# Kernel optimization log

Measured on AMD Instinct MI355X. Metric: run time of the kernel, lower is better.

Reference implementation:

```python
import jax, jax.numpy as jnp
import numpy as np

N, E, G = 50000, 800000, 128
F_IN, H, NHID, C = 310, 128, 64, 2  # H = 2*nhid
NEG_SLOPE = 0.2


def setup_inputs() -> dict:
    key = jax.random.key(0)
    ks = jax.random.split(key, 16)
    def lin(k, fan_in, shape):
        return (jax.random.normal(k, shape, jnp.float32) / np.sqrt(fan_in)).astype(jnp.float32)
    return {
        "x": jax.random.normal(ks[0], (N, F_IN), jnp.float32),
        "edge_index": jax.random.randint(ks[1], (2, E), 0, N, dtype=jnp.int32),
        "batch": jnp.sort(jax.random.randint(ks[2], (N,), 0, G, dtype=jnp.int32)),
        "W1": lin(ks[3], F_IN, (F_IN, H)),
        "a_src1": lin(ks[4], H, (H,)),
        "a_dst1": lin(ks[5], H, (H,)),
        "b1": jnp.zeros((H,), jnp.float32),
        "W2": lin(ks[6], H, (H, H)),
        "a_src2": lin(ks[7], H, (H,)),
        "a_dst2": lin(ks[8], H, (H,)),
        "b2": jnp.zeros((H,), jnp.float32),
        "fc1_w": lin(ks[9], H, (H, NHID)),
        "fc1_b": jnp.zeros((NHID,), jnp.float32),
        "fc2_w": lin(ks[10], NHID, (NHID, C)),
        "fc2_b": jnp.zeros((C,), jnp.float32),
    }


def _gat(x, src, dst, W, a_src, a_dst, b):
    # PyG GATConv, heads=1: h = xW; e_ij = LeakyReLU(a_src.h_j + a_dst.h_i)
    h = x @ W                               # [N, H]
    asrc = h @ a_src                        # [N]
    adst = h @ a_dst                        # [N]
    e = jax.nn.leaky_relu(asrc[src] + adst[dst], NEG_SLOPE)  # [E']
    # segment softmax over incoming edges of each target node
    m = jax.ops.segment_max(e, dst, num_segments=N)
    ex = jnp.exp(e - m[dst])
    s = jax.ops.segment_sum(ex, dst, num_segments=N)
    w = ex / s[dst]                         # [E']
    out = jax.ops.segment_sum(h[src] * w[:, None], dst, num_segments=N)
    return out + b


def reference(x, edge_index, batch, W1, a_src1, a_dst1, b1,
              W2, a_src2, a_dst2, b2, fc1_w, fc1_b, fc2_w, fc2_b):
    # add self loops (GATConv default add_self_loops=True)
    ar = jnp.arange(N, dtype=edge_index.dtype)
    src = jnp.concatenate([edge_index[0], ar])
    dst = jnp.concatenate([edge_index[1], ar])

    h = jax.nn.selu(_gat(x, src, dst, W1, a_src1, a_dst1, b1))
    h = jax.nn.selu(_gat(h, src, dst, W2, a_src2, a_dst2, b2))

    # global mean pool over graphs
    summed = jax.ops.segment_sum(h, batch, num_segments=G)          # [G, H]
    cnt = jax.ops.segment_sum(jnp.ones((N,), h.dtype), batch, num_segments=G)
    pooled = jax.nn.selu(summed / jnp.maximum(cnt, 1.0)[:, None])

    z = jax.nn.selu(pooled @ fc1_w + fc1_b)  # dropout is identity in eval
    logits = z @ fc2_w + fc2_b
    return jax.nn.log_softmax(logits, axis=-1)
```

## Files before the change

kernel.cpp:

```cpp
#include <hip/hip_runtime.h>
#include <hip/hip_bf16.h>
#include <math.h>

#define NN 50000
#define NE 800000
#define NET (NE + NN)
#define FIN 310
#define HD 128
#define NHID 64
#define NCLS 2
#define NG 128
#define NEG_SLOPE 0.2f
#define KP1 320
#define KP2 128

#define SLOTS 64
#define NPART 8
#define PART_SZ (NN / NPART)
#define EPB 4096
#define NSLICE ((NET + EPB - 1) / EPB)

#define SELU_SCALE 1.0507009873554804934193349852946f
#define SELU_ALPHA 1.6732632423543772848170429916717f

typedef short bf16x8 __attribute__((ext_vector_type(8)));
typedef float f32x4 __attribute__((ext_vector_type(4)));

__device__ __forceinline__ float selu(float x) {
    return SELU_SCALE * (x > 0.f ? x : SELU_ALPHA * (expf(x) - 1.f));
}
__device__ __forceinline__ float lrelu(float x) {
    return x > 0.f ? x : NEG_SLOPE * x;
}
__device__ __forceinline__ unsigned short f2bf(float f) {
    unsigned int u = __float_as_uint(f);
    u = (u + 0x7fffu + ((u >> 16) & 1u)) >> 16;
    return (unsigned short)u;
}
__device__ __forceinline__ float bf2f(unsigned short b) {
    return __uint_as_float(((unsigned int)b) << 16);
}


__global__ __launch_bounds__(256) void k_scatter_slots(const int* __restrict__ ei,
                                                       int* __restrict__ cursor,
                                                       int* __restrict__ slots) {
    int part = blockIdx.x & (NPART - 1);
    int slice = blockIdx.x >> 3;
    int lo = part * PART_SZ;
    int base = slice * EPB + threadIdx.x;
#pragma unroll
    for (int k = 0; k < EPB / 256; ++k) {
        int i = base + k * 256;
        if (i >= NET) break;
        int d = (i < NE) ? ei[NE + i] : (i - NE);
        if ((unsigned)(d - lo) < (unsigned)PART_SZ) {
            int s = (i < NE) ? ei[i] : d;
            int pos = atomicAdd(&cursor[d], 1) & (SLOTS - 1);
            slots[(size_t)d * SLOTS + pos] = s;
        }
    }
}


__global__ void k_castT2(const float* __restrict__ W1, const float* __restrict__ W2,
                         unsigned short* __restrict__ W1t, unsigned short* __restrict__ W2t) {
    int i = blockIdx.x * blockDim.x + threadIdx.x;
    const int N1 = HD * KP1;
    if (i < N1) {
        int n = i / KP1, k = i % KP1;
        W1t[i] = (k < FIN) ? f2bf(W1[(size_t)k * HD + n]) : (unsigned short)0;
    } else {
        int j = i - N1;
        if (j < HD * KP2) {
            int n = j / KP2, k = j % KP2;
            W2t[j] = f2bf(W2[(size_t)k * HD + n]);
        }
    }
}


#define GEMM_EPILOGUE                                                          \
    int gr_base = r0 + w * 16 + quad * 4;                                      \
    _Pragma("unroll")                                                          \
    for (int r = 0; r < 4; ++r) {                                              \
        int gr = gr_base + r;                                                  \
        if (gr < M) {                                                          \
            _Pragma("unroll")                                                  \
            for (int nt = 0; nt < 8; ++nt)                                     \
                C[(size_t)gr * HD + nt * 16 + l16] = f2bf(acc[nt][r]);         \
        }                                                                      \
    }                                                                          \
    _Pragma("unroll")                                                          \
    for (int r = 0; r < 4; ++r) {                                              \
        float s1 = 0.f, s2 = 0.f;                                              \
        _Pragma("unroll")                                                      \
        for (int nt = 0; nt < 8; ++nt) {                                       \
            int c = nt * 16 + l16;                                             \
            float v = acc[nt][r];                                              \
            s1 += v * a1s[c];                                                  \
            s2 += v * a2s[c];                                                  \
        }                                                                      \
        _Pragma("unroll")                                                      \
        for (int off = 1; off < 16; off <<= 1) {                               \
            s1 += __shfl_xor(s1, off);                                         \
            s2 += __shfl_xor(s2, off);                                         \
        }                                                                      \
        int gr = gr_base + r;                                                  \
        if (l16 == 0 && gr < M) { asrcp[gr] = s1; adstp[gr] = s2; }            \
    }

__global__ __launch_bounds__(256) void k_gemm_f32(const float* __restrict__ A,
                                                  const unsigned short* __restrict__ Bt,
                                                  unsigned short* __restrict__ C,
                                                  float* __restrict__ asrcp,
                                                  float* __restrict__ adstp,
                                                  const float* __restrict__ a_src,
                                                  const float* __restrict__ a_dst,
                                                  int M, int K, int Kp) {
    __shared__ unsigned short As[64][40];
    __shared__ unsigned short Bs[128][40];
    __shared__ float a1s[HD], a2s[HD];
    int t = threadIdx.x;
    int lane = t & 63, w = t >> 6;
    int quad = lane >> 4, l16 = lane & 15;
    int r0 = blockIdx.x * 64;

    if (t < HD) a1s[t] = a_src[t];
    else a2s[t - HD] = a_dst[t - HD];

    f32x4 acc[8] = {};
    int arow = t >> 4;
    int acol = (t & 15) * 2;
    int brow = t >> 1;
    int bcol = (t & 1) * 16;

    for (int k0 = 0; k0 < Kp; k0 += 32) {
#pragma unroll
        for (int p = 0; p < 4; ++p) {
            int rl = arow + p * 16;
            int gr = r0 + rl;
            int gk = k0 + acol;
            float2 v = make_float2(0.f, 0.f);
            if (gr < M) {
                if (gk + 1 < K) v = *(const float2*)(A + (size_t)gr * K + gk);
                else if (gk < K) v.x = A[(size_t)gr * K + gk];
            }
            ushort2 b;
            b.x = f2bf(v.x); b.y = f2bf(v.y);
            *(ushort2*)&As[rl][acol] = b;
        }
        {
            const unsigned short* src = Bt + (size_t)brow * Kp + k0 + bcol;
            uint4 u0 = *(const uint4*)(src);
            uint4 u1 = *(const uint4*)(src + 8);
            *(uint4*)&Bs[brow][bcol] = u0;
            *(uint4*)&Bs[brow][bcol + 8] = u1;
        }
        __syncthreads();
        bf16x8 af = *(bf16x8*)&As[w * 16 + l16][quad * 8];
#pragma unroll
        for (int nt = 0; nt < 8; ++nt) {
            bf16x8 bfr = *(bf16x8*)&Bs[nt * 16 + l16][quad * 8];
            acc[nt] = __builtin_amdgcn_mfma_f32_16x16x32_bf16(af, bfr, acc[nt], 0, 0, 0);
        }
        __syncthreads();
    }
    GEMM_EPILOGUE
}

__global__ __launch_bounds__(256) void k_gemm_bf16(const unsigned short* __restrict__ A,
                                                   const unsigned short* __restrict__ Bt,
                                                   unsigned short* __restrict__ C,
                                                   float* __restrict__ asrcp,
                                                   float* __restrict__ adstp,
                                                   const float* __restrict__ a_src,
                                                   const float* __restrict__ a_dst,
                                                   int M, int K, int Kp) {
    __shared__ unsigned short As[64][40];
    __shared__ unsigned short Bs[128][40];
    __shared__ float a1s[HD], a2s[HD];
    int t = threadIdx.x;
    int lane = t & 63, w = t >> 6;
    int quad = lane >> 4, l16 = lane & 15;
    int r0 = blockIdx.x * 64;

    if (t < HD) a1s[t] = a_src[t];
    else a2s[t - HD] = a_dst[t - HD];

    f32x4 acc[8] = {};
    int arow = t >> 2;
    int acol = (t & 3) * 8;
    int brow = t >> 1;
    int bcol = (t & 1) * 16;

    for (int k0 = 0; k0 < Kp; k0 += 32) {
        {
            int gr = r0 + arow;
            uint4 v = make_uint4(0, 0, 0, 0);
            if (gr < M) v = *(const uint4*)(A + (size_t)gr * K + k0 + acol);
            *(uint4*)&As[arow][acol] = v;
        }
        {
            const unsigned short* src = Bt + (size_t)brow * Kp + k0 + bcol;
            uint4 u0 = *(const uint4*)(src);
            uint4 u1 = *(const uint4*)(src + 8);
            *(uint4*)&Bs[brow][bcol] = u0;
            *(uint4*)&Bs[brow][bcol + 8] = u1;
        }
        __syncthreads();
        bf16x8 af = *(bf16x8*)&As[w * 16 + l16][quad * 8];
#pragma unroll
        for (int nt = 0; nt < 8; ++nt) {
            bf16x8 bfr = *(bf16x8*)&Bs[nt * 16 + l16][quad * 8];
            acc[nt] = __builtin_amdgcn_mfma_f32_16x16x32_bf16(af, bfr, acc[nt], 0, 0, 0);
        }
        __syncthreads();
    }
    GEMM_EPILOGUE
}


__global__ __launch_bounds__(256) void k_gat(const unsigned short* __restrict__ h,
                                             const float* __restrict__ asrc,
                                             const float* __restrict__ adst,
                                             const int* __restrict__ degv,
                                             const int* __restrict__ slots,
                                             const float* __restrict__ bias,
                                             unsigned short* __restrict__ out) {
    int node = blockIdx.x * 4 + (threadIdx.x >> 6);
    int lane = threadIdx.x & 63;
    if (node >= NN) return;
    int g = lane >> 4, cl = lane & 15;
    int deg = degv[node];
    float adsti = adst[node];

    float acc[8] = {0.f, 0.f, 0.f, 0.f, 0.f, 0.f, 0.f, 0.f};

    int cnt = min(deg, SLOTS);
    int s_c = 0; float p_c = 0.f;
    if (lane < cnt) {
        s_c = slots[(size_t)node * SLOTS + lane];
        p_c = __expf(lrelu(asrc[s_c] + adsti));
    }
    float den_l = p_c;
    int nt = (cnt + 3) >> 2;
    for (int t = 0; t < nt; t += 4) {
        float pv[4]; uint4 hv[4];
#pragma unroll
        for (int u = 0; u < 4; ++u) {
            int tt = t + u;
            bool valid = tt < nt;
            int e = (4 * tt + g) & 63;
            int s = __shfl(s_c, e);
            float p = __shfl(p_c, e);
            int sa = valid ? s : 0;
            pv[u] = valid ? p : 0.f;
            hv[u] = *(const uint4*)(h + (size_t)sa * HD + cl * 8);
        }
#pragma unroll
        for (int u = 0; u < 4; ++u) {
            float p = pv[u];
            unsigned int w0 = hv[u].x, w1 = hv[u].y, w2 = hv[u].z, w3 = hv[u].w;
            acc[0] += p * __uint_as_float(w0 << 16);
            acc[1] += p * __uint_as_float(w0 & 0xffff0000u);
            acc[2] += p * __uint_as_float(w1 << 16);
            acc[3] += p * __uint_as_float(w1 & 0xffff0000u);
            acc[4] += p * __uint_as_float(w2 << 16);
            acc[5] += p * __uint_as_float(w2 & 0xffff0000u);
            acc[6] += p * __uint_as_float(w3 << 16);
            acc[7] += p * __uint_as_float(w3 & 0xffff0000u);
        }
    }
#pragma unroll
    for (int k = 0; k < 8; ++k) {
        acc[k] += __shfl_xor(acc[k], 16);
        acc[k] += __shfl_xor(acc[k], 32);
    }
#pragma unroll
    for (int off = 32; off; off >>= 1)
        den_l += __shfl_xor(den_l, off);

    if (g == 0) {
        float inv = 1.f / den_l;
        int c0 = cl * 8;
        float4 b0 = *(const float4*)(bias + c0);
        float4 b1 = *(const float4*)(bias + c0 + 4);
        float v0 = selu(acc[0] * inv + b0.x);
        float v1 = selu(acc[1] * inv + b0.y);
        float v2 = selu(acc[2] * inv + b0.z);
        float v3 = selu(acc[3] * inv + b0.w);
        float v4 = selu(acc[4] * inv + b1.x);
        float v5 = selu(acc[5] * inv + b1.y);
        float v6 = selu(acc[6] * inv + b1.z);
        float v7 = selu(acc[7] * inv + b1.w);
        uint4 pk;
        pk.x = (unsigned int)f2bf(v0) | ((unsigned int)f2bf(v1) << 16);
        pk.y = (unsigned int)f2bf(v2) | ((unsigned int)f2bf(v3) << 16);
        pk.z = (unsigned int)f2bf(v4) | ((unsigned int)f2bf(v5) << 16);
        pk.w = (unsigned int)f2bf(v6) | ((unsigned int)f2bf(v7) << 16);
        *(uint4*)(out + (size_t)node * HD + c0) = pk;
    }
}


__device__ __forceinline__ int lower_bound_i(const int* a, int n, int key) {
    int lo = 0, hi = n;
    while (lo < hi) {
        int mid = (lo + hi) >> 1;
        if (a[mid] < key) lo = mid + 1; else hi = mid;
    }
    return lo;
}

__global__ __launch_bounds__(512) void k_poolfc(const unsigned short* __restrict__ x,
                                                const int* __restrict__ batch,
                                                const float* __restrict__ w1,
                                                const float* __restrict__ b1,
                                                const float* __restrict__ w2,
                                                const float* __restrict__ b2,
                                                float* __restrict__ out) {
    int g = blockIdx.x;
    int t = threadIdx.x;
    __shared__ int lo_s, hi_s;
    __shared__ float red[512];
    __shared__ float pooled_s[128];
    if (t == 0) {
        lo_s = lower_bound_i(batch, NN, g);
        hi_s = lower_bound_i(batch, NN, g + 1);
    }
    __syncthreads();
    int lo = lo_s, hi = hi_s;
    float acc = 0.f;
    for (int n = lo + (t >> 7); n < hi; n += 4)
        acc += bf2f(x[(size_t)n * HD + (t & 127)]);
    red[t] = acc;
    __syncthreads();
    if (t < 128) {
        float v = red[t] + red[t + 128] + red[t + 256] + red[t + 384];
        pooled_s[t] = selu(v / fmaxf((float)(hi - lo), 1.f));
    }
    __syncthreads();
    if (t < 64) {
        float z = 0.f;
#pragma unroll 8
        for (int k = 0; k < HD; ++k) z += pooled_s[k] * w1[k * NHID + t];
        z = selu(z + b1[t]);
        float p0 = z * w2[t * NCLS + 0];
        float p1 = z * w2[t * NCLS + 1];
        for (int off = 32; off; off >>= 1) {
            p0 += __shfl_down(p0, off);
            p1 += __shfl_down(p1, off);
        }
        if (t == 0) {
            float l0 = p0 + b2[0], l1 = p1 + b2[1];
            float m = fmaxf(l0, l1);
            float lse = m + logf(expf(l0 - m) + expf(l1 - m));
            out[g * NCLS + 0] = l0 - lse;
            out[g * NCLS + 1] = l1 - lse;
        }
    }
}


static inline size_t align_up(size_t v, size_t a) { return (v + a - 1) / a * a; }

extern "C" void kernel_launch(void* const* d_in, const int* in_sizes, int n_in,
                              void* d_out, int out_size, void* d_ws, size_t ws_size,
                              hipStream_t stream) {
    const float* x      = (const float*)d_in[0];
    const int*   ei     = (const int*)d_in[1];
    const int*   batch  = (const int*)d_in[2];
    const float* W1     = (const float*)d_in[3];
    const float* a_src1 = (const float*)d_in[4];
    const float* a_dst1 = (const float*)d_in[5];
    const float* b1     = (const float*)d_in[6];
    const float* W2     = (const float*)d_in[7];
    const float* a_src2 = (const float*)d_in[8];
    const float* a_dst2 = (const float*)d_in[9];
    const float* b2     = (const float*)d_in[10];
    const float* fc1_w  = (const float*)d_in[11];
    const float* fc1_b  = (const float*)d_in[12];
    const float* fc2_w  = (const float*)d_in[13];
    const float* fc2_b  = (const float*)d_in[14];
    float* out = (float*)d_out;

    char* ws = (char*)d_ws;
    size_t off = 0;
    unsigned short* h1 = (unsigned short*)(ws + off); off = align_up(off + (size_t)NN * HD * 2, 256);
    unsigned short* o1 = (unsigned short*)(ws + off); off = align_up(off + (size_t)NN * HD * 2, 256);
    float* asrc = (float*)(ws + off); off = align_up(off + (size_t)NN * 4, 256);
    float* adst = (float*)(ws + off); off = align_up(off + (size_t)NN * 4, 256);
    int* cursor = (int*)(ws + off);   off = align_up(off + (size_t)NN * 4, 256);
    int* slots  = (int*)(ws + off);   off = align_up(off + (size_t)NN * SLOTS * 4, 256);
    unsigned short* W1t = (unsigned short*)(ws + off); off = align_up(off + (size_t)HD * KP1 * 2, 256);
    unsigned short* W2t = (unsigned short*)(ws + off); off = align_up(off + (size_t)HD * KP2 * 2, 256);
    (void)ws_size;

    hipMemsetAsync(cursor, 0, (size_t)NN * 4, stream);
    k_scatter_slots<<<NSLICE * NPART, 256, 0, stream>>>(ei, cursor, slots);

    k_castT2<<<(HD * (KP1 + KP2) + 255) / 256, 256, 0, stream>>>(W1, W2, W1t, W2t);

    int gblocks = (NN + 63) / 64;

    k_gemm_f32<<<gblocks, 256, 0, stream>>>(x, W1t, h1, asrc, adst, a_src1, a_dst1, NN, FIN, KP1);
    k_gat<<<(NN + 3) / 4, 256, 0, stream>>>(h1, asrc, adst, cursor, slots, b1, o1);

    k_gemm_bf16<<<gblocks, 256, 0, stream>>>(o1, W2t, h1, asrc, adst, a_src2, a_dst2, NN, HD, KP2);
    k_gat<<<(NN + 3) / 4, 256, 0, stream>>>(h1, asrc, adst, cursor, slots, b2, o1);

    k_poolfc<<<NG, 512, 0, stream>>>(o1, batch, fc1_w, fc1_b, fc2_w, fc2_b, out);
}
```

Baseline: 315.1 us.

## Shrink GEMM row tile, split columns across waves, narrow GAT unroll, fast math

The GEMM kernels now handle 32 rows per block instead of 64. Each of the four waves covers a 16-row by 64-column quadrant, and the attention dot products are reduced through shared memory. This doubles the block count and halves the accumulator registers, which should raise occupancy. The cost is that each B tile is reused across fewer rows and each block pays an extra barrier. The GAT gather loop is also unrolled by 2 instead of 4 with float2 accumulators, and selu/log-softmax switch to fast __expf/__logf intrinsics, trading a little precision.

```diff
diff --git a/kernel.cpp b/kernel.cpp
--- a/kernel.cpp
+++ b/kernel.cpp
@@ -27,7 +27,7 @@
 typedef float f32x4 __attribute__((ext_vector_type(4)));
 
 __device__ __forceinline__ float selu(float x) {
-    return SELU_SCALE * (x > 0.f ? x : SELU_ALPHA * (expf(x) - 1.f));
+    return SELU_SCALE * (x > 0.f ? x : SELU_ALPHA * (__expf(x) - 1.f));
 }
 __device__ __forceinline__ float lrelu(float x) {
     return x > 0.f ? x : NEG_SLOPE * x;
@@ -81,22 +81,23 @@
 
 
 #define GEMM_EPILOGUE                                                          \
-    int gr_base = r0 + w * 16 + quad * 4;                                      \
+    int rh = w & 1, chf = w >> 1;                                              \
+    int gr_base = r0 + rh * 16 + quad * 4;                                     \
     _Pragma("unroll")                                                          \
     for (int r = 0; r < 4; ++r) {                                              \
         int gr = gr_base + r;                                                  \
         if (gr < M) {                                                          \
             _Pragma("unroll")                                                  \
-            for (int nt = 0; nt < 8; ++nt)                                     \
-                C[(size_t)gr * HD + nt * 16 + l16] = f2bf(acc[nt][r]);         \
+            for (int nt = 0; nt < 4; ++nt)                                     \
+                C[(size_t)gr * HD + chf * 64 + nt * 16 + l16] = f2bf(acc[nt][r]); \
         }                                                                      \
     }                                                                          \
     _Pragma("unroll")                                                          \
     for (int r = 0; r < 4; ++r) {                                              \
         float s1 = 0.f, s2 = 0.f;                                              \
         _Pragma("unroll")                                                      \
-        for (int nt = 0; nt < 8; ++nt) {                                       \
-            int c = nt * 16 + l16;                                             \
+        for (int nt = 0; nt < 4; ++nt) {                                       \
+            int c = chf * 64 + nt * 16 + l16;                                  \
             float v = acc[nt][r];                                              \
             s1 += v * a1s[c];                                                  \
             s2 += v * a2s[c];                                                  \
@@ -106,8 +107,19 @@
             s1 += __shfl_xor(s1, off);                                         \
             s2 += __shfl_xor(s2, off);                                         \
         }                                                                      \
-        int gr = gr_base + r;                                                  \
-        if (l16 == 0 && gr < M) { asrcp[gr] = s1; adstp[gr] = s2; }            \
+        if (l16 == 0) {                                                        \
+            pd[0][rh][chf][quad * 4 + r] = s1;                                 \
+            pd[1][rh][chf][quad * 4 + r] = s2;                                 \
+        }                                                                      \
+    }                                                                          \
+    __syncthreads();                                                           \
+    if (t < 64) {                                                              \
+        int idx = t & 15;                                                      \
+        int rh2 = (t >> 4) & 1;                                                \
+        int which = t >> 5;                                                    \
+        float val = pd[which][rh2][0][idx] + pd[which][rh2][1][idx];           \
+        int gr = r0 + rh2 * 16 + idx;                                          \
+        if (gr < M) { if (which) adstp[gr] = val; else asrcp[gr] = val; }      \
     }
 
 __global__ __launch_bounds__(256) void k_gemm_f32(const float* __restrict__ A,
@@ -118,18 +130,19 @@
                                                   const float* __restrict__ a_src,
                                                   const float* __restrict__ a_dst,
                                                   int M, int K, int Kp) {
-    __shared__ unsigned short As[64][40];
+    __shared__ unsigned short As[32][40];
     __shared__ unsigned short Bs[128][40];
     __shared__ float a1s[HD], a2s[HD];
+    __shared__ float pd[2][2][2][16];
     int t = threadIdx.x;
     int lane = t & 63, w = t >> 6;
     int quad = lane >> 4, l16 = lane & 15;
-    int r0 = blockIdx.x * 64;
+    int r0 = blockIdx.x * 32;
 
     if (t < HD) a1s[t] = a_src[t];
     else a2s[t - HD] = a_dst[t - HD];
 
-    f32x4 acc[8] = {};
+    f32x4 acc[4] = {};
     int arow = t >> 4;
     int acol = (t & 15) * 2;
     int brow = t >> 1;
@@ -137,7 +150,7 @@
 
     for (int k0 = 0; k0 < Kp; k0 += 32) {
 #pragma unroll
-        for (int p = 0; p < 4; ++p) {
+        for (int p = 0; p < 2; ++p) {
             int rl = arow + p * 16;
             int gr = r0 + rl;
             int gk = k0 + acol;
@@ -158,10 +171,10 @@
             *(uint4*)&Bs[brow][bcol + 8] = u1;
         }
         __syncthreads();
-        bf16x8 af = *(bf16x8*)&As[w * 16 + l16][quad * 8];
-#pragma unroll
-        for (int nt = 0; nt < 8; ++nt) {
-            bf16x8 bfr = *(bf16x8*)&Bs[nt * 16 + l16][quad * 8];
+        bf16x8 af = *(bf16x8*)&As[(w & 1) * 16 + l16][quad * 8];
+#pragma unroll
+        for (int nt = 0; nt < 4; ++nt) {
+            bf16x8 bfr = *(bf16x8*)&Bs[(w >> 1) * 64 + nt * 16 + l16][quad * 8];
             acc[nt] = __builtin_amdgcn_mfma_f32_16x16x32_bf16(af, bfr, acc[nt], 0, 0, 0);
         }
         __syncthreads();
@@ -177,29 +190,30 @@
                                                    const float* __restrict__ a_src,
                                                    const float* __restrict__ a_dst,
                                                    int M, int K, int Kp) {
-    __shared__ unsigned short As[64][40];
+    __shared__ unsigned short As[32][40];
     __shared__ unsigned short Bs[128][40];
     __shared__ float a1s[HD], a2s[HD];
+    __shared__ float pd[2][2][2][16];
     int t = threadIdx.x;
     int lane = t & 63, w = t >> 6;
     int quad = lane >> 4, l16 = lane & 15;
-    int r0 = blockIdx.x * 64;
+    int r0 = blockIdx.x * 32;
 
     if (t < HD) a1s[t] = a_src[t];
     else a2s[t - HD] = a_dst[t - HD];
 
-    f32x4 acc[8] = {};
-    int arow = t >> 2;
-    int acol = (t & 3) * 8;
+    f32x4 acc[4] = {};
+    int arow = t >> 3;
+    int acol = (t & 7) * 4;
     int brow = t >> 1;
     int bcol = (t & 1) * 16;
 
     for (int k0 = 0; k0 < Kp; k0 += 32) {
         {
             int gr = r0 + arow;
-            uint4 v = make_uint4(0, 0, 0, 0);
-            if (gr < M) v = *(const uint4*)(A + (size_t)gr * K + k0 + acol);
-            *(uint4*)&As[arow][acol] = v;
+            uint2 v = make_uint2(0, 0);
+            if (gr < M) v = *(const uint2*)(A + (size_t)gr * K + k0 + acol);
+            *(uint2*)&As[arow][acol] = v;
         }
         {
             const unsigned short* src = Bt + (size_t)brow * Kp + k0 + bcol;
@@ -209,10 +223,10 @@
             *(uint4*)&Bs[brow][bcol + 8] = u1;
         }
         __syncthreads();
-        bf16x8 af = *(bf16x8*)&As[w * 16 + l16][quad * 8];
-#pragma unroll
-        for (int nt = 0; nt < 8; ++nt) {
-            bf16x8 bfr = *(bf16x8*)&Bs[nt * 16 + l16][quad * 8];
+        bf16x8 af = *(bf16x8*)&As[(w & 1) * 16 + l16][quad * 8];
+#pragma unroll
+        for (int nt = 0; nt < 4; ++nt) {
+            bf16x8 bfr = *(bf16x8*)&Bs[(w >> 1) * 64 + nt * 16 + l16][quad * 8];
             acc[nt] = __builtin_amdgcn_mfma_f32_16x16x32_bf16(af, bfr, acc[nt], 0, 0, 0);
         }
         __syncthreads();
@@ -235,7 +249,7 @@
     int deg = degv[node];
     float adsti = adst[node];
 
-    float acc[8] = {0.f, 0.f, 0.f, 0.f, 0.f, 0.f, 0.f, 0.f};
+    float2 acc2[4] = {};
 
     int cnt = min(deg, SLOTS);
     int s_c = 0; float p_c = 0.f;
@@ -245,10 +259,10 @@
     }
     float den_l = p_c;
     int nt = (cnt + 3) >> 2;
-    for (int t = 0; t < nt; t += 4) {
-        float pv[4]; uint4 hv[4];
-#pragma unroll
-        for (int u = 0; u < 4; ++u) {
+    for (int t = 0; t < nt; t += 2) {
+        float pv[2]; uint4 hv[2];
+#pragma unroll
+        for (int u = 0; u < 2; ++u) {
             int tt = t + u;
             bool valid = tt < nt;
             int e = (4 * tt + g) & 63;
@@ -259,23 +273,25 @@
             hv[u] = *(const uint4*)(h + (size_t)sa * HD + cl * 8);
         }
 #pragma unroll
-        for (int u = 0; u < 4; ++u) {
+        for (int u = 0; u < 2; ++u) {
             float p = pv[u];
             unsigned int w0 = hv[u].x, w1 = hv[u].y, w2 = hv[u].z, w3 = hv[u].w;
-            acc[0] += p * __uint_as_float(w0 << 16);
-            acc[1] += p * __uint_as_float(w0 & 0xffff0000u);
-            acc[2] += p * __uint_as_float(w1 << 16);
-            acc[3] += p * __uint_as_float(w1 & 0xffff0000u);
-            acc[4] += p * __uint_as_float(w2 << 16);
-            acc[5] += p * __uint_as_float(w2 & 0xffff0000u);
-            acc[6] += p * __uint_as_float(w3 << 16);
-            acc[7] += p * __uint_as_float(w3 & 0xffff0000u);
-        }
-    }
-#pragma unroll
-    for (int k = 0; k < 8; ++k) {
-        acc[k] += __shfl_xor(acc[k], 16);
-        acc[k] += __shfl_xor(acc[k], 32);
+            acc2[0].x += p * __uint_as_float(w0 << 16);
+            acc2[0].y += p * __uint_as_float(w0 & 0xffff0000u);
+            acc2[1].x += p * __uint_as_float(w1 << 16);
+            acc2[1].y += p * __uint_as_float(w1 & 0xffff0000u);
+            acc2[2].x += p * __uint_as_float(w2 << 16);
+            acc2[2].y += p * __uint_as_float(w2 & 0xffff0000u);
+            acc2[3].x += p * __uint_as_float(w3 << 16);
+            acc2[3].y += p * __uint_as_float(w3 & 0xffff0000u);
+        }
+    }
+#pragma unroll
+    for (int k = 0; k < 4; ++k) {
+        acc2[k].x += __shfl_xor(acc2[k].x, 16);
+        acc2[k].y += __shfl_xor(acc2[k].y, 16);
+        acc2[k].x += __shfl_xor(acc2[k].x, 32);
+        acc2[k].y += __shfl_xor(acc2[k].y, 32);
     }
 #pragma unroll
     for (int off = 32; off; off >>= 1)
@@ -286,14 +302,14 @@
         int c0 = cl * 8;
         float4 b0 = *(const float4*)(bias + c0);
         float4 b1 = *(const float4*)(bias + c0 + 4);
-        float v0 = selu(acc[0] * inv + b0.x);
-        float v1 = selu(acc[1] * inv + b0.y);
-        float v2 = selu(acc[2] * inv + b0.z);
-        float v3 = selu(acc[3] * inv + b0.w);
-        float v4 = selu(acc[4] * inv + b1.x);
-        float v5 = selu(acc[5] * inv + b1.y);
-        float v6 = selu(acc[6] * inv + b1.z);
-        float v7 = selu(acc[7] * inv + b1.w);
+        float v0 = selu(acc2[0].x * inv + b0.x);
+        float v1 = selu(acc2[0].y * inv + b0.y);
+        float v2 = selu(acc2[1].x * inv + b0.z);
+        float v3 = selu(acc2[1].y * inv + b0.w);
+        float v4 = selu(acc2[2].x * inv + b1.x);
+        float v5 = selu(acc2[2].y * inv + b1.y);
+        float v6 = selu(acc2[3].x * inv + b1.z);
+        float v7 = selu(acc2[3].y * inv + b1.w);
         uint4 pk;
         pk.x = (unsigned int)f2bf(v0) | ((unsigned int)f2bf(v1) << 16);
         pk.y = (unsigned int)f2bf(v2) | ((unsigned int)f2bf(v3) << 16);
@@ -355,7 +371,7 @@
         if (t == 0) {
             float l0 = p0 + b2[0], l1 = p1 + b2[1];
             float m = fmaxf(l0, l1);
-            float lse = m + logf(expf(l0 - m) + expf(l1 - m));
+            float lse = m + __logf(__expf(l0 - m) + __expf(l1 - m));
             out[g * NCLS + 0] = l0 - lse;
             out[g * NCLS + 1] = l1 - lse;
         }
@@ -402,7 +418,7 @@
 
     k_castT2<<<(HD * (KP1 + KP2) + 255) / 256, 256, 0, stream>>>(W1, W2, W1t, W2t);
 
-    int gblocks = (NN + 63) / 64;
+    int gblocks = (NN + 31) / 32;
 
     k_gemm_f32<<<gblocks, 256, 0, stream>>>(x, W1t, h1, asrc, adst, a_src1, a_dst1, NN, FIN, KP1);
     k_gat<<<(NN + 3) / 4, 256, 0, stream>>>(h1, asrc, adst, cursor, slots, b1, o1);
```

Result: no change. 309.1 us (-1.9%).
